# Kernel optimization log

Measured on AMD Instinct MI355X. Metric: run time of the kernel, lower is better.

The kernel has to match this reference:

```python
import jax, jax.numpy as jnp
import numpy as np

HEAD_SIZE = 64


def setup_inputs() -> dict:
    key = jax.random.key(0)
    ks = jax.random.split(key, 10)
    B, S, D, H, hs = 4, 2048, 768, 12, HEAD_SIZE
    F = 4 * D
    sd = lambda n: 1.0 / np.sqrt(n)
    return {
        "x": jax.random.normal(ks[0], (B, S, D), jnp.float32),
        "Wq": jax.random.normal(ks[1], (H, D, hs), jnp.float32) * sd(D),
        "Wk": jax.random.normal(ks[2], (H, D, hs), jnp.float32) * sd(D),
        "Wv": jax.random.normal(ks[3], (H, D, hs), jnp.float32) * sd(D),
        "Wo": jax.random.normal(ks[4], (D, D), jnp.float32) * sd(D),
        "bo": jnp.zeros((D,), jnp.float32),
        "W1": jax.random.normal(ks[5], (D, F), jnp.float32) * sd(D),
        "b1": jnp.zeros((F,), jnp.float32),
        "W2": jax.random.normal(ks[6], (F, D), jnp.float32) * sd(F),
        "b2": jnp.zeros((D,), jnp.float32),
    }


def reference(x, Wq, Wk, Wv, Wo, bo, W1, b1, W2, b2):
    B, S, D = x.shape
    hs = Wq.shape[-1]
    # per-head projections (no bias), vectorized over heads: [B,H,S,hs]
    q = jnp.einsum("bsd,hde->bhse", x, Wq)
    k = jnp.einsum("bsd,hde->bhse", x, Wk)
    v = jnp.einsum("bsd,hde->bhse", x, Wv)
    # causal attention scores [B,H,S,S], scaled by sqrt(head_size)
    scores = jnp.einsum("bhse,bhte->bhst", q, k) / jnp.sqrt(jnp.float32(hs))
    causal = jnp.tril(jnp.ones((S, S), dtype=bool))
    scores = jnp.where(causal, scores, -jnp.inf)
    attn = jax.nn.softmax(scores, axis=-1)
    z = jnp.einsum("bhst,bhte->bhse", attn, v)
    # concat heads along feature dim (head order preserved) -> [B,S,D]
    z = z.transpose(0, 2, 1, 3).reshape(B, S, D)
    # output projection + residual
    z = z @ Wo + bo + x
    # FFN + residual
    h = jax.nn.relu(z @ W1 + b1)
    return h @ W2 + b2 + z
```

## Files before the change

### kernel.cpp

```cpp
#include <hip/hip_runtime.h>


typedef __attribute__((ext_vector_type(4))) float f32x4;
typedef __attribute__((ext_vector_type(8))) short bf16x8;
typedef __attribute__((ext_vector_type(4))) unsigned short u16x4;

#define GLB_AS __attribute__((address_space(1)))
#define LDS_AS __attribute__((address_space(3)))

__device__ __forceinline__ unsigned short f2bf(float f) {
  unsigned int u = __float_as_uint(f);
  u = (u + 0x7FFFu + ((u >> 16) & 1u)) >> 16;
  return (unsigned short)u;
}

__device__ __forceinline__ void gload16(const void* g, void* l) {
  __builtin_amdgcn_global_load_lds((const GLB_AS unsigned int*)g,
                                   (LDS_AS unsigned int*)l, 16, 0, 0);
}

__device__ __forceinline__ int xcd_swz(int orig, int nwg) {
  int q = nwg >> 3, r = nwg & 7;
  int xcd = orig & 7, rest = orig >> 3;
  return (xcd < r ? xcd * (q + 1) : r * (q + 1) + (xcd - r) * q) + rest;
}

__global__ void castx(const float* __restrict__ in, unsigned short* __restrict__ out, int n) {
  int i = (blockIdx.x * 256 + threadIdx.x) * 4;
  if (i < n) {
    float4 f = *(const float4*)&in[i];
    u16x4 o;
    o[0] = f2bf(f.x); o[1] = f2bf(f.y); o[2] = f2bf(f.z); o[3] = f2bf(f.w);
    *(u16x4*)&out[i] = o;
  }
}

__global__ void tcast(const float* __restrict__ in, unsigned short* __restrict__ out,
                      int R, int C, float scale) {
  __shared__ float tile[32][33];
  const float* inb = in + (size_t)blockIdx.z * R * C;
  unsigned short* outb = out + (size_t)blockIdx.z * R * C;
  int bx = blockIdx.x * 32;
  int by = blockIdx.y * 32;
  int tx = threadIdx.x, ty = threadIdx.y;
  #pragma unroll
  for (int i = 0; i < 32; i += 8) {
    int r = by + ty + i, c = bx + tx;
    tile[ty + i][tx] = inb[(size_t)r * C + c];
  }
  __syncthreads();
  #pragma unroll
  for (int i = 0; i < 32; i += 8) {
    int c = bx + ty + i, r = by + tx;
    outb[(size_t)c * R + r] = f2bf(tile[tx][ty + i] * scale);
  }
}

__global__ void tcast3(const float* __restrict__ Wq, const float* __restrict__ Wk,
                       const float* __restrict__ Wv, unsigned short* __restrict__ out,
                       float qscale) {
  __shared__ float tile[32][33];
  const int R = 768, C = 64;
  int z = blockIdx.z, wsel = z / 12, head = z % 12;
  const float* in = (wsel == 0 ? Wq : wsel == 1 ? Wk : Wv) + (size_t)head * R * C;
  unsigned short* outb = out + (size_t)wsel * R * R + (size_t)head * R * C;
  float scale = wsel == 0 ? qscale : 1.0f;
  int bx = blockIdx.x * 32;
  int by = blockIdx.y * 32;
  int tx = threadIdx.x, ty = threadIdx.y;
  #pragma unroll
  for (int i = 0; i < 32; i += 8)
    tile[ty + i][tx] = in[(size_t)(by + ty + i) * C + bx + tx];
  __syncthreads();
  #pragma unroll
  for (int i = 0; i < 32; i += 8)
    outb[(size_t)(bx + ty + i) * R + by + tx] = f2bf(tile[tx][ty + i] * scale);
}

__global__ void vtrans(const unsigned short* __restrict__ v, unsigned short* __restrict__ vT) {
  __shared__ unsigned short tile[32][33];
  int bh = blockIdx.z, b = bh / 12, h = bh % 12;
  int s0 = blockIdx.x * 32, e0 = blockIdx.y * 32;
  int tx = threadIdx.x, ty = threadIdx.y;
  #pragma unroll
  for (int i = 0; i < 32; i += 8)
    tile[ty + i][tx] = v[(size_t)(b * 2048 + s0 + ty + i) * 768 + h * 64 + e0 + tx];
  __syncthreads();
  #pragma unroll
  for (int i = 0; i < 32; i += 8)
    vT[(size_t)((b * 12 + h) * 64 + e0 + ty + i) * 2048 + s0 + tx] = tile[tx][ty + i];
}

template <int EPI>
__global__ void gemm_bf16(const unsigned short* __restrict__ A,
                          const unsigned short* __restrict__ Bt,
                          const float* __restrict__ bias,
                          const float* __restrict__ resid,
                          float* __restrict__ Cf,
                          unsigned short* __restrict__ Cb,
                          int M, int N, int K, int gy, size_t segN) {
  __shared__ unsigned short Alds[2][128 * 32];
  __shared__ unsigned short Blds[2][128 * 32];
  const int tid = threadIdx.x;
  const int lane = tid & 63;
  const int w = tid >> 6;
  const int wm = w & 1, wn = w >> 1;
  const int wg = xcd_swz(blockIdx.x, gridDim.x);
  const int gsz = 8 * gy;
  const int group = wg / gsz;
  const int rem = wg - group * gsz;
  const int bm = (group * 8 + (rem & 7)) * 128;
  const int bn = (rem >> 3) * 128;

  f32x4 acc[4][4] = {};

  const int r0 = tid >> 2;
  const int c0 = (tid & 3) * 8;

  #pragma unroll
  for (int i = 0; i < 2; ++i) {
    int row = r0 + i * 64;
    gload16(&A[(size_t)(bm + row) * K + c0], &Alds[0][row * 32 + c0]);
    gload16(&Bt[(size_t)(bn + row) * K + c0], &Blds[0][row * 32 + c0]);
  }
  __syncthreads();

  int buf = 0;
  for (int k0 = 0; k0 < K; k0 += 32) {
    if (k0 + 32 < K) {
      #pragma unroll
      for (int i = 0; i < 2; ++i) {
        int row = r0 + i * 64;
        gload16(&A[(size_t)(bm + row) * K + k0 + 32 + c0], &Alds[buf ^ 1][row * 32 + c0]);
        gload16(&Bt[(size_t)(bn + row) * K + k0 + 32 + c0], &Blds[buf ^ 1][row * 32 + c0]);
      }
    }
    bf16x8 af[4], bf[4];
    #pragma unroll
    for (int m = 0; m < 4; ++m)
      af[m] = *(const bf16x8*)&Alds[buf][(wm * 64 + m * 16 + (lane & 15)) * 32 + (lane >> 4) * 8];
    #pragma unroll
    for (int n = 0; n < 4; ++n)
      bf[n] = *(const bf16x8*)&Blds[buf][(wn * 64 + n * 16 + (lane & 15)) * 32 + (lane >> 4) * 8];
    #pragma unroll
    for (int m = 0; m < 4; ++m)
      #pragma unroll
      for (int n = 0; n < 4; ++n)
        acc[m][n] = __builtin_amdgcn_mfma_f32_16x16x32_bf16(af[m], bf[n], acc[m][n], 0, 0, 0);
    __syncthreads();
    buf ^= 1;
  }

  const int crow0 = bm + wm * 64 + (lane >> 4) * 4;
  const int ccol0 = bn + wn * 64 + (lane & 15);
  const int seg = bn / 768;
  const int lcol0 = (bn % 768) + wn * 64 + (lane & 15);
  #pragma unroll
  for (int m = 0; m < 4; ++m) {
    #pragma unroll
    for (int n = 0; n < 4; ++n) {
      int col = ccol0 + n * 16;
      #pragma unroll
      for (int r = 0; r < 4; ++r) {
        int row = crow0 + m * 16 + r;
        float v = acc[m][n][r];
        if constexpr (EPI & 1) v += bias[col];
        if constexpr (EPI & 4) v += resid[(size_t)row * N + col];
        if constexpr (EPI & 2) v = fmaxf(v, 0.f);
        if constexpr (EPI & 8) Cf[(size_t)row * N + col] = v;
        if constexpr (EPI & 16) Cb[(size_t)row * N + col] = f2bf(v);
        if constexpr (EPI & 32)
          Cb[(size_t)seg * segN + (size_t)row * 768 + lcol0 + n * 16] = f2bf(v);
      }
    }
  }
}

__global__ void attn_fwd(const unsigned short* __restrict__ q,
                         const unsigned short* __restrict__ k,
                         const unsigned short* __restrict__ vT,
                         unsigned short* __restrict__ z) {
  __shared__ unsigned short Klds[2 * 2 * 64 * 32];
  __shared__ unsigned short Vlds[2 * 2 * 64 * 32];
  __shared__ unsigned short Plds[4 * 16 * 72];

  const int wgid = xcd_swz(blockIdx.x, gridDim.x);
  const int pi = wgid & 15;
  const int bh = wgid >> 4;
  const int b = bh / 12, h = bh % 12;
  const int tid = threadIdx.x, lane = tid & 63, w = tid >> 6;
  const int q16 = lane & 15;
  const int qt  = lane >> 4;
  const int rdc = ((qt ^ (lane & 3)) * 8);

  const int srow = tid >> 2;
  const int sdc  = (tid & 3) * 8;
  const int sgc  = (((tid & 3) ^ (srow & 3)) * 8);
  const size_t kbase = (size_t)(b * 2048) * 768 + h * 64;
  const size_t vbase = (size_t)((b * 12 + h) * 64) * 2048;
  unsigned short* Pw = &Plds[w * 16 * 72];

  #pragma unroll 1
  for (int seg = 0; seg < 2; ++seg) {
    const int qb = seg == 0 ? pi : 31 - pi;
    const int q0 = qb * 64;
    const int nt = qb + 1;

    const int qrow = q0 + w * 16 + q16;
    const size_t qoff = (size_t)(b * 2048 + qrow) * 768 + h * 64 + qt * 8;
    bf16x8 qf0 = *(const bf16x8*)&q[qoff];
    bf16x8 qf1 = *(const bf16x8*)&q[qoff + 32];

    f32x4 accO[4] = {};
    float mrow = -3.0e38f, lrow = 0.f;

    #pragma unroll
    for (int i = 0; i < 2; ++i) {
      gload16(&k[kbase + (size_t)srow * 768 + i * 32 + sgc],
              &Klds[i * 2048 + srow * 32 + sdc]);
      gload16(&vT[vbase + (size_t)srow * 2048 + i * 32 + sgc],
              &Vlds[i * 2048 + srow * 32 + sdc]);
    }
    __syncthreads();

    int buf = 0;
    for (int t = 0; t < nt; ++t) {
      if (t + 1 < nt) {
        const int kv1 = (t + 1) * 64;
        const int bo = (buf ^ 1) * 4096;
        #pragma unroll
        for (int i = 0; i < 2; ++i) {
          gload16(&k[kbase + (size_t)(kv1 + srow) * 768 + i * 32 + sgc],
                  &Klds[bo + i * 2048 + srow * 32 + sdc]);
          gload16(&vT[vbase + (size_t)srow * 2048 + kv1 + i * 32 + sgc],
                  &Vlds[bo + i * 2048 + srow * 32 + sdc]);
        }
      }

      const int kv0 = t * 64;
      const int kb_ = buf * 4096;

      f32x4 s[4];
      #pragma unroll
      for (int n = 0; n < 4; ++n) {
        bf16x8 kf0 = *(const bf16x8*)&Klds[kb_ + 0 * 2048 + (n * 16 + q16) * 32 + rdc];
        bf16x8 kf1 = *(const bf16x8*)&Klds[kb_ + 1 * 2048 + (n * 16 + q16) * 32 + rdc];
        f32x4 acc0 = {};
        acc0 = __builtin_amdgcn_mfma_f32_16x16x32_bf16(kf0, qf0, acc0, 0, 0, 0);
        s[n] = __builtin_amdgcn_mfma_f32_16x16x32_bf16(kf1, qf1, acc0, 0, 0, 0);
      }

      if (t == nt - 1) {
        const int rowg = q0 + w * 16 + q16;
        #pragma unroll
        for (int n = 0; n < 4; ++n)
          #pragma unroll
          for (int r = 0; r < 4; ++r)
            if (kv0 + n * 16 + qt * 4 + r > rowg) s[n][r] = -3.0e38f;
      }

      float pm = s[0][0];
      #pragma unroll
      for (int n = 0; n < 4; ++n)
        #pragma unroll
        for (int r = 0; r < 4; ++r) pm = fmaxf(pm, s[n][r]);
      pm = fmaxf(pm, __shfl_xor(pm, 16));
      pm = fmaxf(pm, __shfl_xor(pm, 32));

      if (__any(pm > mrow + 8.f)) {
        float mnew = fmaxf(mrow, pm);
        float sc = exp2f(mrow - mnew);
        mrow = mnew;
        lrow *= sc;
        int isc = __float_as_int(sc);
        #pragma unroll
        for (int r = 0; r < 4; ++r) {
          float scr = __int_as_float(__builtin_amdgcn_ds_bpermute((qt * 4 + r) * 4, isc));
          #pragma unroll
          for (int n = 0; n < 4; ++n) accO[n][r] *= scr;
        }
      }

      float psum = 0.f;
      #pragma unroll
      for (int n = 0; n < 4; ++n)
        #pragma unroll
        for (int r = 0; r < 4; ++r) { s[n][r] = exp2f(s[n][r] - mrow); psum += s[n][r]; }
      psum += __shfl_xor(psum, 16);
      psum += __shfl_xor(psum, 32);
      lrow += psum;

      #pragma unroll
      for (int n = 0; n < 4; ++n) {
        unsigned int lo, hi;
        asm("v_cvt_pk_bf16_f32 %0, %1, %2" : "=v"(lo) : "v"(s[n][0]), "v"(s[n][1]));
        asm("v_cvt_pk_bf16_f32 %0, %1, %2" : "=v"(hi) : "v"(s[n][2]), "v"(s[n][3]));
        uint2 pk; pk.x = lo; pk.y = hi;
        *(uint2*)&Pw[q16 * 72 + n * 16 + qt * 4] = pk;
      }

      #pragma unroll
      for (int kk = 0; kk < 2; ++kk) {
        bf16x8 pf = *(const bf16x8*)&Pw[q16 * 72 + kk * 32 + qt * 8];
        #pragma unroll
        for (int n = 0; n < 4; ++n) {
          bf16x8 vf = *(const bf16x8*)&Vlds[kb_ + kk * 2048 + (n * 16 + q16) * 32 + rdc];
          accO[n] = __builtin_amdgcn_mfma_f32_16x16x32_bf16(pf, vf, accO[n], 0, 0, 0);
        }
      }

      __syncthreads();
      buf ^= 1;
    }

    #pragma unroll
    for (int r = 0; r < 4; ++r) {
      float lr = __int_as_float(__builtin_amdgcn_ds_bpermute((qt * 4 + r) * 4,
                                                             __float_as_int(lrow)));
      float linv = 1.0f / lr;
      int rowg = q0 + w * 16 + qt * 4 + r;
      #pragma unroll
      for (int n = 0; n < 4; ++n)
        z[(size_t)(b * 2048 + rowg) * 768 + h * 64 + n * 16 + q16]
            = f2bf(accO[n][r] * linv);
    }
  }
}

extern "C" void kernel_launch(void* const* d_in, const int* in_sizes, int n_in,
                              void* d_out, int out_size, void* d_ws, size_t ws_size,
                              hipStream_t stream) {
  const float* x  = (const float*)d_in[0];
  const float* Wq = (const float*)d_in[1];
  const float* Wk = (const float*)d_in[2];
  const float* Wv = (const float*)d_in[3];
  const float* Wo = (const float*)d_in[4];
  const float* bo = (const float*)d_in[5];
  const float* W1 = (const float*)d_in[6];
  const float* b1 = (const float*)d_in[7];
  const float* W2 = (const float*)d_in[8];
  const float* b2 = (const float*)d_in[9];
  float* out = (float*)d_out;

  const int B = 4, S = 2048, D = 768, H = 12, hs = 64, F = 3072;
  const int M = B * S;
  const size_t MD = (size_t)M * D;

  unsigned short* xb   = (unsigned short*)d_ws;
  unsigned short* qb   = xb + MD;
  unsigned short* kb   = qb + MD;
  unsigned short* vb   = kb + MD;
  unsigned short* hbuf = xb;
  unsigned short* vT   = vb + MD;
  unsigned short* zb   = vT + MD;
  float*          z2f  = (float*)(zb + MD);
  unsigned short* z2b  = (unsigned short*)(z2f + MD);
  unsigned short* wqkvT= z2b + MD;
  unsigned short* woT  = wqkvT + 3 * (size_t)D * D;
  unsigned short* w1T  = woT + (size_t)D * D;
  unsigned short* w2T  = w1T + (size_t)D * F;

  dim3 tb(32, 8);

  castx<<<dim3((int)(MD / 4 / 256)), 256, 0, stream>>>(x, xb, (int)MD);

  const float QS = 0.125f * 1.4426950408889634f;
  tcast3<<<dim3(hs / 32, D / 32, 3 * H), tb, 0, stream>>>(Wq, Wk, Wv, wqkvT, QS);
  tcast<<<dim3(D / 32, D / 32, 1), tb, 0, stream>>>(Wo, woT, D, D, 1.0f);
  tcast<<<dim3(F / 32, D / 32, 1), tb, 0, stream>>>(W1, w1T, D, F, 1.0f);
  tcast<<<dim3(D / 32, F / 32, 1), tb, 0, stream>>>(W2, w2T, F, D, 1.0f);

  {
    int gy = 3 * D / 128;
    gemm_bf16<32><<<dim3(64 * gy), 256, 0, stream>>>(xb, wqkvT, nullptr, nullptr,
                                                     nullptr, qb, M, 3 * D, D, gy, MD);
  }

  vtrans<<<dim3(S / 32, hs / 32, B * H), tb, 0, stream>>>(vb, vT);

  attn_fwd<<<dim3((S / 128) * B * H), 256, 0, stream>>>(qb, kb, vT, zb);

  {
    int gy = D / 128;
    gemm_bf16<1 | 4 | 8 | 16><<<dim3(64 * gy), 256, 0, stream>>>(zb, woT, bo, x,
                                                                 z2f, z2b, M, D, D, gy, 0);
  }
  {
    int gy = F / 128;
    gemm_bf16<1 | 2 | 16><<<dim3(64 * gy), 256, 0, stream>>>(z2b, w1T, b1, nullptr,
                                                             nullptr, hbuf, M, F, D, gy, 0);
  }
  {
    int gy = D / 128;
    gemm_bf16<1 | 4 | 8><<<dim3(64 * gy), 256, 0, stream>>>(hbuf, w2T, b2, z2f,
                                                            out, nullptr, M, D, F, gy, 0);
  }
}
```

Measured before the change: 288.6 us.

## Add 256x256 ping-pong pipelined GEMM for QKV and FFN1, tune attention swizzle and priority

Introduces a new 512-thread 256x256-tile bf16 GEMM with double-buffered LDS, direct global-to-LDS loads interleaved with MFMA phases, explicit vmcnt waits, barriers and s_setprio around MFMA blocks. It is used for the QKV projection and the first FFN GEMM. The goal is more data reuse per tile and better overlap of loads with math. The attention kernel gets a changed LDS XOR swizzle to cut bank conflicts, plus setprio around its MFMA loops. Larger tiles reduce the number of workgroups and raise register and LDS pressure, which risks lower occupancy or wave-quantization losses.

```diff
diff --git a/kernel.cpp b/kernel.cpp
--- a/kernel.cpp
+++ b/kernel.cpp
@@ -44,16 +44,12 @@
   int by = blockIdx.y * 32;
   int tx = threadIdx.x, ty = threadIdx.y;
   #pragma unroll
-  for (int i = 0; i < 32; i += 8) {
-    int r = by + ty + i, c = bx + tx;
-    tile[ty + i][tx] = inb[(size_t)r * C + c];
-  }
+  for (int i = 0; i < 32; i += 8)
+    tile[ty + i][tx] = inb[(size_t)(by + ty + i) * C + bx + tx];
   __syncthreads();
   #pragma unroll
-  for (int i = 0; i < 32; i += 8) {
-    int c = bx + ty + i, r = by + tx;
-    outb[(size_t)c * R + r] = f2bf(tile[tx][ty + i] * scale);
-  }
+  for (int i = 0; i < 32; i += 8)
+    outb[(size_t)(bx + ty + i) * R + by + tx] = f2bf(tile[tx][ty + i] * scale);
 }
 
 __global__ void tcast3(const float* __restrict__ Wq, const float* __restrict__ Wk,
@@ -151,10 +147,8 @@
     buf ^= 1;
   }
 
-  const int crow0 = bm + wm * 64 + (lane >> 4) * 4;
+  const int crow0 = bm + wm * 64 + ((lane >> 4)) * 4;
   const int ccol0 = bn + wn * 64 + (lane & 15);
-  const int seg = bn / 768;
-  const int lcol0 = (bn % 768) + wn * 64 + (lane & 15);
   #pragma unroll
   for (int m = 0; m < 4; ++m) {
     #pragma unroll
@@ -169,8 +163,154 @@
         if constexpr (EPI & 2) v = fmaxf(v, 0.f);
         if constexpr (EPI & 8) Cf[(size_t)row * N + col] = v;
         if constexpr (EPI & 16) Cb[(size_t)row * N + col] = f2bf(v);
+      }
+    }
+  }
+}
+
+#define RDA4(AR, b, mf0, mf1)                                              \
+  AR[0] = *(const bf16x8*)&lds[b][0][aBase + (mf0)*1024 + sc0];            \
+  AR[1] = *(const bf16x8*)&lds[b][0][aBase + (mf0)*1024 + sc1];            \
+  AR[2] = *(const bf16x8*)&lds[b][0][aBase + (mf1)*1024 + sc0];            \
+  AR[3] = *(const bf16x8*)&lds[b][0][aBase + (mf1)*1024 + sc1];
+
+#define RDB8(BR, b)                                                        \
+  _Pragma("unroll") for (int nf = 0; nf < 4; ++nf) {                       \
+    BR[nf*2+0] = *(const bf16x8*)&lds[b][1][bBase + nf*1024 + sc0];        \
+    BR[nf*2+1] = *(const bf16x8*)&lds[b][1][bBase + nf*1024 + sc1];        \
+  }
+
+#define MFMA16(mp, AR, BR)                                                 \
+  __builtin_amdgcn_s_setprio(1);                                           \
+  _Pragma("unroll") for (int mi = 0; mi < 2; ++mi)                         \
+    _Pragma("unroll") for (int nf = 0; nf < 4; ++nf) {                     \
+      acc[(mp)+mi][nf] = __builtin_amdgcn_mfma_f32_16x16x32_bf16(          \
+          AR[mi*2+0], BR[nf*2+0], acc[(mp)+mi][nf], 0, 0, 0);              \
+      acc[(mp)+mi][nf] = __builtin_amdgcn_mfma_f32_16x16x32_bf16(          \
+          AR[mi*2+1], BR[nf*2+1], acc[(mp)+mi][nf], 0, 0, 0);              \
+    }                                                                      \
+  __builtin_amdgcn_s_setprio(0);
+
+#define STG(b, X, h, kt) {                                                 \
+    const unsigned short* _s = (X) ? Bt : A;                               \
+    const size_t _rb = (X) ? (size_t)bn : (size_t)bm;                      \
+    _Pragma("unroll") for (int _l = 0; _l < 2; ++_l) {                     \
+      int _r = (h)*128 + _l*64 + s_row;                                    \
+      gload16(&_s[(_rb + _r) * K + (kt)*64 + s_gc8],                       \
+              &lds[b][X][_r*64 + s_sc8]);                                  \
+    } }
+
+#define PHX() { __builtin_amdgcn_sched_barrier(0); __builtin_amdgcn_s_barrier(); }
+
+template <int EPI>
+__global__ __launch_bounds__(512, 2)
+void gemm256(const unsigned short* __restrict__ A,
+             const unsigned short* __restrict__ Bt,
+             const float* __restrict__ bias,
+             const float* __restrict__ resid,
+             float* __restrict__ Cf,
+             unsigned short* __restrict__ Cb,
+             int M, int N, int K, int gy, size_t segN) {
+  __shared__ unsigned short lds[2][2][16384];
+  const int tid = threadIdx.x;
+  const int lane = tid & 63;
+  const int w = tid >> 6;
+  const int wr = w >> 2, wc = w & 3;
+  const int q16 = lane & 15, qt = lane >> 4;
+
+  const int wg = xcd_swz(blockIdx.x, gridDim.x);
+  const int gsz = 4 * gy;
+  const int group = wg / gsz;
+  const int rem = wg - group * gsz;
+  const int bm = (group * 4 + (rem & 3)) * 256;
+  const int bn = (rem >> 2) * 256;
+
+  const int s_row = tid >> 3;
+  const int s_sc  = tid & 7;
+  const int s_sc8 = s_sc * 8;
+  const int s_gc8 = (s_sc ^ (s_row & 7)) * 8;
+
+  const int aBase = (wr * 128 + q16) * 64;
+  const int bBase = (wc * 64 + q16) * 64;
+  const int sc0 = ((qt) ^ (q16 & 7)) * 8;
+  const int sc1 = ((4 + qt) ^ (q16 & 7)) * 8;
+
+  f32x4 acc[8][4] = {};
+  bf16x8 Aa[4], Ab[4], Ba[8], Bb[8];
+
+  const int nt = K >> 6;
+
+  STG(0, 0, 0, 0) STG(0, 0, 1, 0) STG(0, 1, 0, 0) STG(0, 1, 1, 0)
+  STG(1, 1, 0, 1) STG(1, 1, 1, 1) STG(1, 0, 0, 1)
+  asm volatile("s_waitcnt vmcnt(6)" ::: "memory");
+  __builtin_amdgcn_s_barrier();
+  RDB8(Ba, 0)
+  RDA4(Aa, 0, 0, 1)
+  PHX();
+
+  for (int t = 0; t < nt; t += 2) {
+    const bool s2 = (t + 2 < nt), s3 = (t + 3 < nt);
+    RDA4(Ab, 0, 2, 3)
+    MFMA16(0, Aa, Ba)
+    STG(1, 0, 1, t + 1)
+    if (s2) STG(0, 1, 0, t + 2)
+    PHX();
+    RDA4(Aa, 0, 4, 5)
+    MFMA16(2, Ab, Ba)
+    if (s2) STG(0, 1, 1, t + 2)
+    PHX();
+    RDA4(Ab, 0, 6, 7)
+    MFMA16(4, Aa, Ba)
+    if (s2) { asm volatile("s_waitcnt vmcnt(4)" ::: "memory"); }
+    else    { asm volatile("s_waitcnt vmcnt(0)" ::: "memory"); }
+    PHX();
+    RDB8(Bb, 1)
+    RDA4(Aa, 1, 0, 1)
+    MFMA16(6, Ab, Ba)
+    if (s2) STG(0, 0, 0, t + 2)
+    PHX();
+    RDA4(Ab, 1, 2, 3)
+    MFMA16(0, Aa, Bb)
+    if (s2) STG(0, 0, 1, t + 2)
+    if (s3) STG(1, 1, 0, t + 3)
+    PHX();
+    RDA4(Aa, 1, 4, 5)
+    MFMA16(2, Ab, Bb)
+    if (s3) STG(1, 1, 1, t + 3)
+    PHX();
+    RDA4(Ab, 1, 6, 7)
+    MFMA16(4, Aa, Bb)
+    asm volatile("s_waitcnt vmcnt(4)" ::: "memory");
+    PHX();
+    if (s2) {
+      RDB8(Ba, 0)
+      RDA4(Aa, 0, 0, 1)
+    }
+    MFMA16(6, Ab, Bb)
+    if (s3) STG(1, 0, 0, t + 3)
+    PHX();
+  }
+
+  const int crow0 = bm + wr * 128 + qt * 4;
+  const int ccol0 = bn + wc * 64 + q16;
+  const int seg = bn / 768;
+  const int lcol0 = (bn % 768) + wc * 64 + q16;
+  #pragma unroll
+  for (int mf = 0; mf < 8; ++mf) {
+    #pragma unroll
+    for (int nf = 0; nf < 4; ++nf) {
+      int col = ccol0 + nf * 16;
+      #pragma unroll
+      for (int j = 0; j < 4; ++j) {
+        int row = crow0 + mf * 16 + j;
+        float v = acc[mf][nf][j];
+        if constexpr (EPI & 1) v += bias[col];
+        if constexpr (EPI & 4) v += resid[(size_t)row * N + col];
+        if constexpr (EPI & 2) v = fmaxf(v, 0.f);
+        if constexpr (EPI & 8) Cf[(size_t)row * N + col] = v;
+        if constexpr (EPI & 16) Cb[(size_t)row * N + col] = f2bf(v);
         if constexpr (EPI & 32)
-          Cb[(size_t)seg * segN + (size_t)row * 768 + lcol0 + n * 16] = f2bf(v);
+          Cb[(size_t)seg * segN + (size_t)row * 768 + lcol0 + nf * 16] = f2bf(v);
       }
     }
   }
@@ -191,11 +331,11 @@
   const int tid = threadIdx.x, lane = tid & 63, w = tid >> 6;
   const int q16 = lane & 15;
   const int qt  = lane >> 4;
-  const int rdc = ((qt ^ (lane & 3)) * 8);
+  const int rdc = ((qt ^ ((q16 >> 1) & 3)) * 8);
 
   const int srow = tid >> 2;
   const int sdc  = (tid & 3) * 8;
-  const int sgc  = (((tid & 3) ^ (srow & 3)) * 8);
+  const int sgc  = (((tid & 3) ^ ((srow >> 1) & 3)) * 8);
   const size_t kbase = (size_t)(b * 2048) * 768 + h * 64;
   const size_t vbase = (size_t)((b * 12 + h) * 64) * 2048;
   unsigned short* Pw = &Plds[w * 16 * 72];
@@ -241,6 +381,7 @@
       const int kb_ = buf * 4096;
 
       f32x4 s[4];
+      __builtin_amdgcn_s_setprio(1);
       #pragma unroll
       for (int n = 0; n < 4; ++n) {
         bf16x8 kf0 = *(const bf16x8*)&Klds[kb_ + 0 * 2048 + (n * 16 + q16) * 32 + rdc];
@@ -249,6 +390,7 @@
         acc0 = __builtin_amdgcn_mfma_f32_16x16x32_bf16(kf0, qf0, acc0, 0, 0, 0);
         s[n] = __builtin_amdgcn_mfma_f32_16x16x32_bf16(kf1, qf1, acc0, 0, 0, 0);
       }
+      __builtin_amdgcn_s_setprio(0);
 
       if (t == nt - 1) {
         const int rowg = q0 + w * 16 + q16;
@@ -299,6 +441,7 @@
         *(uint2*)&Pw[q16 * 72 + n * 16 + qt * 4] = pk;
       }
 
+      __builtin_amdgcn_s_setprio(1);
       #pragma unroll
       for (int kk = 0; kk < 2; ++kk) {
         bf16x8 pf = *(const bf16x8*)&Pw[q16 * 72 + kk * 32 + qt * 8];
@@ -308,6 +451,7 @@
           accO[n] = __builtin_amdgcn_mfma_f32_16x16x32_bf16(pf, vf, accO[n], 0, 0, 0);
         }
       }
+      __builtin_amdgcn_s_setprio(0);
 
       __syncthreads();
       buf ^= 1;
@@ -371,9 +515,9 @@
   tcast<<<dim3(D / 32, F / 32, 1), tb, 0, stream>>>(W2, w2T, F, D, 1.0f);
 
   {
-    int gy = 3 * D / 128;
-    gemm_bf16<32><<<dim3(64 * gy), 256, 0, stream>>>(xb, wqkvT, nullptr, nullptr,
-                                                     nullptr, qb, M, 3 * D, D, gy, MD);
+    int gy = 3 * D / 256;
+    gemm256<32><<<dim3((M / 256) * gy), 512, 0, stream>>>(xb, wqkvT, nullptr, nullptr,
+                                                          nullptr, qb, M, 3 * D, D, gy, MD);
   }
 
   vtrans<<<dim3(S / 32, hs / 32, B * H), tb, 0, stream>>>(vb, vT);
@@ -386,9 +530,9 @@
                                                                  z2f, z2b, M, D, D, gy, 0);
   }
   {
-    int gy = F / 128;
-    gemm_bf16<1 | 2 | 16><<<dim3(64 * gy), 256, 0, stream>>>(z2b, w1T, b1, nullptr,
-                                                             nullptr, hbuf, M, F, D, gy, 0);
+    int gy = F / 256;
+    gemm256<1 | 2 | 16><<<dim3((M / 256) * gy), 512, 0, stream>>>(z2b, w1T, b1, nullptr,
+                                                                  nullptr, hbuf, M, F, D, gy, 0);
   }
   {
     int gy = D / 128;
```

New measurement: 430.9 us. 49.3% more time.
